# Kernel optimization log

Hardware: AMD Instinct MI355X
Metric: run time of the kernel (lower is better)

Reference implementation:

```python
import jax, jax.numpy as jnp
import numpy as np

LN_EPS = 1e-5  # torch LayerNorm default


def layer_norm(x, g, b):
    mu = jnp.mean(x, axis=-1, keepdims=True)
    var = jnp.mean((x - mu) ** 2, axis=-1, keepdims=True)
    return (x - mu) / jnp.sqrt(var + LN_EPS) * g + b


def setup_inputs() -> dict:
    key = jax.random.key(0)
    k0, k1 = jax.random.split(key, 2)
    B, C, N, T, D = 64, 2, 1024, 13, 256  # batch, in_dim, nodes, time_step+1, dim
    x = jax.random.normal(k0, (B, C, N, T), dtype=jnp.float32)
    conv_w = jax.random.normal(k1, (D, C, T), dtype=jnp.float32) * 0.05  # Conv2d kernel (1,T) squeezed
    conv_b = jnp.zeros((D,), dtype=jnp.float32)
    time_g = jnp.ones((D,), dtype=jnp.float32)
    time_b = jnp.zeros((D,), dtype=jnp.float32)
    static_g = jnp.ones((N,), dtype=jnp.float32)
    static_b = jnp.zeros((N,), dtype=jnp.float32)
    return {"x": x, "conv_w": conv_w, "conv_b": conv_b,
            "time_g": time_g, "time_b": time_b,
            "static_g": static_g, "static_b": static_b}


def reference(x, conv_w, conv_b, time_g, time_b, static_g, static_b):
    # Conv2d(in_dim, dim, kernel=(1, T)) on [B,C,N,T] -> [B,dim,N,1]; squeeze+transpose -> [B,N,dim]
    emb = jnp.einsum('bcnt,dct->bnd', x, conv_w) + conv_b
    emb = layer_norm(emb, time_g, time_b)  # [B, N, D]
    # Spearman rank correlation, batched (replaces Python loop over B)
    ranks = jnp.argsort(jnp.argsort(emb, axis=-1), axis=-1).astype(emb.dtype)  # [B,N,D]
    c = ranks - jnp.mean(ranks, axis=-1, keepdims=True)
    norm = jnp.sqrt(jnp.sum(c * c, axis=-1, keepdims=True))  # [B,N,1]
    corr = jnp.einsum('bnd,bmd->bnm', c, c)  # [B,N,N]
    adj = jnp.abs(corr / (norm * jnp.swapaxes(norm, -1, -2) + 1e-8))
    # LayerNorm over last (nodes) axis then ReLU
    return jax.nn.relu(layer_norm(adj, static_g, static_b))
```

## Files before the change

### kernel.cpp

```cpp
#include <hip/hip_runtime.h>


typedef __attribute__((ext_vector_type(4))) int i32x4;

__device__ __forceinline__ void load_lds16(const void* g, void* l) {
  __builtin_amdgcn_global_load_lds(
      (const __attribute__((address_space(1))) void*)g,
      (__attribute__((address_space(3))) void*)l, 16, 0, 0);
}

__global__ __launch_bounds__(256) void conv_rank_kernel(
    const float* __restrict__ x, const float* __restrict__ w,
    const float* __restrict__ cb, const float* __restrict__ tg,
    const float* __restrict__ tb, signed char* __restrict__ ranks)
{
  int grp = blockIdx.x;
  int b = grp >> 8;
  int n0 = (grp & 255) << 2;
  int tid = threadIdx.x;
  int wave = tid >> 6, lane = tid & 63;
  int row = b * 1024 + n0 + wave;

  __shared__ float xs[4][26];
  __shared__ unsigned int ws[4][256];

  if (tid < 104) {
    int c = tid / 52, rem = tid - c * 52;
    int r = rem / 13, t = rem - r * 13;
    xs[r][c * 13 + t] = x[((size_t)(b * 2 + c) * 1024 + n0 + r) * 13 + t];
  }
  __syncthreads();

  float accv[4];
  #pragma unroll
  for (int i = 0; i < 4; ++i) {
    int d = i * 64 + lane;
    const float2* wp = (const float2*)(w + d * 26);
    float a = cb[d];
    #pragma unroll
    for (int u = 0; u < 13; ++u) {
      float2 w2 = wp[u];
      a += w2.x * xs[wave][2 * u] + w2.y * xs[wave][2 * u + 1];
    }
    accv[i] = a;
  }

  float s1 = accv[0] + accv[1] + accv[2] + accv[3];
  float s2 = accv[0] * accv[0] + accv[1] * accv[1] +
             accv[2] * accv[2] + accv[3] * accv[3];
  #pragma unroll
  for (int o = 1; o < 64; o <<= 1) {
    s1 += __shfl_xor(s1, o);
    s2 += __shfl_xor(s2, o);
  }
  float mu = s1 * (1.0f / 256.0f);
  float var = s2 * (1.0f / 256.0f) - mu * mu;
  float rs = rsqrtf(var + 1e-5f);

  unsigned int key[4], okey[4];
  #pragma unroll
  for (int i = 0; i < 4; ++i) {
    int d = i * 64 + lane;
    float val = (accv[i] - mu) * rs * tg[d] + tb[d];
    unsigned int u = __float_as_uint(val);
    key[i] = (u & 0x80000000u) ? ~u : (u | 0x80000000u);
    okey[i] = key[i];
  }

  #pragma unroll
  for (int k = 2; k <= 256; k <<= 1) {
    #pragma unroll
    for (int j = k >> 1; j > 0; j >>= 1) {
      if (j < 64) {
        #pragma unroll
        for (int i = 0; i < 4; ++i) {
          unsigned int pk = __shfl_xor(key[i], j);
          int e = i * 64 + lane;
          bool km = ((e & j) == 0) == ((e & k) == 0);
          unsigned int mn = key[i] < pk ? key[i] : pk;
          unsigned int mx = key[i] < pk ? pk : key[i];
          key[i] = km ? mn : mx;
        }
      } else {
        int di = j >> 6;
        #pragma unroll
        for (int i = 0; i < 4; ++i) {
          if ((i & di) == 0) {
            int ip = i + di;
            int e = i * 64 + lane;
            bool up = ((e & k) == 0);
            unsigned int a = key[i], bb = key[ip];
            unsigned int mn = a < bb ? a : bb;
            unsigned int mx = a < bb ? bb : a;
            key[i]  = up ? mn : mx;
            key[ip] = up ? mx : mn;
          }
        }
      }
    }
  }

  #pragma unroll
  for (int i = 0; i < 4; ++i) ws[wave][i * 64 + lane] = key[i];
  __syncthreads();
  int pos[4] = {0, 0, 0, 0};
  #pragma unroll
  for (int s = 128; s > 0; s >>= 1) {
    #pragma unroll
    for (int i = 0; i < 4; ++i)
      pos[i] += (ws[wave][pos[i] + s - 1] < okey[i]) ? s : 0;
  }
  #pragma unroll
  for (int i = 0; i < 4; ++i)
    ranks[(size_t)row * 256 + i * 64 + lane] = (signed char)(pos[i] - 128);
}

__global__ __launch_bounds__(512, 4) void corr_ln_kernel(
    const signed char* __restrict__ ranks, const float* __restrict__ sg,
    const float* __restrict__ sb, float* __restrict__ out)
{
  int bid = blockIdx.x;
  int blk = (bid & 7) * 256 + (bid >> 3);
  int b  = blk >> 5;
  int n0 = (blk & 31) << 5;
  const signed char* R = ranks + (size_t)b * 1024 * 256;
  float* O = out + ((size_t)b * 1024 + n0) * 1024;

  __shared__ __align__(16) signed char As[8192];
  __shared__ __align__(16) signed char Bs[65536];
  __shared__ float red[8][64];
  __shared__ float stats[2][32];

  int tid = threadIdx.x;
  int wave = tid >> 6, lane = tid & 63;
  int fr = lane & 15, quad = lane >> 4;
  int cw = wave << 7;

  {
    int o = tid * 16;
    int kt_a = o >> 11, kq = (o >> 9) & 3, r32 = (o >> 4) & 31;
    load_lds16(R + (size_t)(n0 + r32) * 256 + kt_a * 64 + kq * 16, As + o);
  }

  i32x4 acc[2][8] = {};

  for (int kt = 0; kt < 4; ++kt) {
    #pragma unroll
    for (int i = 0; i < 8; ++i) {
      int o = i * 8192 + tid * 16;
      int kq = o >> 14, row = (o & 16383) >> 4;
      load_lds16(R + (size_t)row * 256 + kt * 64 + kq * 16, Bs + o);
    }
    __syncthreads();

    i32x4 af0 = *(const i32x4*)(As + kt * 2048 + quad * 512 + fr * 16);
    i32x4 af1 = *(const i32x4*)(As + kt * 2048 + quad * 512 + (16 + fr) * 16);
    #pragma unroll
    for (int ni = 0; ni < 8; ++ni) {
      i32x4 bf = *(const i32x4*)(Bs + quad * 16384 + (cw + ni * 16 + fr) * 16);
      acc[0][ni] = __builtin_amdgcn_mfma_i32_16x16x64_i8(af0, bf, acc[0][ni], 0, 0, 0);
      acc[1][ni] = __builtin_amdgcn_mfma_i32_16x16x64_i8(af1, bf, acc[1][ni], 0, 0, 0);
    }
    __syncthreads();
  }

  float nrm = sqrtf(1398080.0f);
  float inv_den = 1.0f / (nrm * nrm + 1e-8f);

  float s[2][4], q[2][4];
  #pragma unroll
  for (int mi = 0; mi < 2; ++mi) {
    #pragma unroll
    for (int v = 0; v < 4; ++v) {
      float ss = 0.0f, qq = 0.0f;
      #pragma unroll
      for (int ni = 0; ni < 8; ++ni) {
        float a = fabsf((float)(acc[mi][ni][v] - 64)) * inv_den;
        ss += a; qq += a * a;
      }
      #pragma unroll
      for (int o = 8; o > 0; o >>= 1) {
        ss += __shfl_xor(ss, o);
        qq += __shfl_xor(qq, o);
      }
      s[mi][v] = ss; q[mi][v] = qq;
    }
  }
  if (fr == 0) {
    #pragma unroll
    for (int mi = 0; mi < 2; ++mi)
      #pragma unroll
      for (int v = 0; v < 4; ++v) {
        int r = mi * 16 + quad * 4 + v;
        red[wave][r] = s[mi][v];
        red[wave][32 + r] = q[mi][v];
      }
  }
  __syncthreads();

  if (tid < 32) {
    float su = 0.0f, sq = 0.0f;
    #pragma unroll
    for (int ww = 0; ww < 8; ++ww) { su += red[ww][tid]; sq += red[ww][32 + tid]; }
    float mu = su * (1.0f / 1024.0f);
    float var = sq * (1.0f / 1024.0f) - mu * mu;
    stats[0][tid] = mu;
    stats[1][tid] = rsqrtf(var + 1e-5f);
  }
  __syncthreads();

  float gv[8], bv[8];
  #pragma unroll
  for (int ni = 0; ni < 8; ++ni) {
    int col = cw + ni * 16 + fr;
    gv[ni] = sg[col];
    bv[ni] = sb[col];
  }
  #pragma unroll
  for (int mi = 0; mi < 2; ++mi) {
    #pragma unroll
    for (int v = 0; v < 4; ++v) {
      int r = mi * 16 + quad * 4 + v;
      float mu = stats[0][r], rs = stats[1][r];
      float* orow = O + (size_t)r * 1024;
      #pragma unroll
      for (int ni = 0; ni < 8; ++ni) {
        float a = fabsf((float)(acc[mi][ni][v] - 64)) * inv_den;
        orow[cw + ni * 16 + fr] = fmaxf(0.0f, (a - mu) * rs * gv[ni] + bv[ni]);
      }
    }
  }
}

extern "C" void kernel_launch(void* const* d_in, const int* in_sizes, int n_in,
                              void* d_out, int out_size, void* d_ws, size_t ws_size,
                              hipStream_t stream) {
  const float* x  = (const float*)d_in[0];
  const float* w  = (const float*)d_in[1];
  const float* cb = (const float*)d_in[2];
  const float* tg = (const float*)d_in[3];
  const float* tb = (const float*)d_in[4];
  const float* sg = (const float*)d_in[5];
  const float* sb = (const float*)d_in[6];
  float* out = (float*)d_out;
  signed char* ranks = (signed char*)d_ws;

  conv_rank_kernel<<<16384, 256, 0, stream>>>(x, w, cb, tg, tb, ranks);
  corr_ln_kernel<<<2048, 512, 0, stream>>>(ranks, sg, sb, out);
}
```

Measured before the change: 529.9 us.

## Sort key-index pairs to scatter ranks directly and swizzle LDS tile layouts

The rank kernel now packs each key with its original index into a 64-bit value and bitonic-sorts the pairs. After sorting, each thread writes the rank straight to the original position, which removes the LDS staging, the barrier and the binary-search pass. The cost is 64-bit shuffles and compares throughout the sort, and scattered byte stores. The correlation kernel changes the As/Bs shared-memory tiles to a row-major layout with an XOR swizzle, so global loads are more contiguous per row and LDS reads hit fewer bank conflicts.

New measurement: 501.7 us. 1.06x faster.

```diff
diff --git a/kernel.cpp b/kernel.cpp
--- a/kernel.cpp
+++ b/kernel.cpp
@@ -22,7 +22,6 @@
   int row = b * 1024 + n0 + wave;
 
   __shared__ float xs[4][26];
-  __shared__ unsigned int ws[4][256];
 
   if (tid < 104) {
     int c = tid / 52, rem = tid - c * 52;
@@ -57,14 +56,14 @@
   float var = s2 * (1.0f / 256.0f) - mu * mu;
   float rs = rsqrtf(var + 1e-5f);
 
-  unsigned int key[4], okey[4];
+  unsigned long long kv[4];
   #pragma unroll
   for (int i = 0; i < 4; ++i) {
     int d = i * 64 + lane;
     float val = (accv[i] - mu) * rs * tg[d] + tb[d];
     unsigned int u = __float_as_uint(val);
-    key[i] = (u & 0x80000000u) ? ~u : (u | 0x80000000u);
-    okey[i] = key[i];
+    unsigned int key = (u & 0x80000000u) ? ~u : (u | 0x80000000u);
+    kv[i] = ((unsigned long long)key << 32) | (unsigned int)d;
   }
 
   #pragma unroll
@@ -74,12 +73,12 @@
       if (j < 64) {
         #pragma unroll
         for (int i = 0; i < 4; ++i) {
-          unsigned int pk = __shfl_xor(key[i], j);
+          unsigned long long p = __shfl_xor(kv[i], j);
           int e = i * 64 + lane;
           bool km = ((e & j) == 0) == ((e & k) == 0);
-          unsigned int mn = key[i] < pk ? key[i] : pk;
-          unsigned int mx = key[i] < pk ? pk : key[i];
-          key[i] = km ? mn : mx;
+          unsigned long long mn = kv[i] < p ? kv[i] : p;
+          unsigned long long mx = kv[i] < p ? p : kv[i];
+          kv[i] = km ? mn : mx;
         }
       } else {
         int di = j >> 6;
@@ -89,30 +88,23 @@
             int ip = i + di;
             int e = i * 64 + lane;
             bool up = ((e & k) == 0);
-            unsigned int a = key[i], bb = key[ip];
-            unsigned int mn = a < bb ? a : bb;
-            unsigned int mx = a < bb ? bb : a;
-            key[i]  = up ? mn : mx;
-            key[ip] = up ? mx : mn;
+            unsigned long long a = kv[i], bb = kv[ip];
+            unsigned long long mn = a < bb ? a : bb;
+            unsigned long long mx = a < bb ? bb : a;
+            kv[i]  = up ? mn : mx;
+            kv[ip] = up ? mx : mn;
           }
         }
       }
     }
   }
 
-  #pragma unroll
-  for (int i = 0; i < 4; ++i) ws[wave][i * 64 + lane] = key[i];
-  __syncthreads();
-  int pos[4] = {0, 0, 0, 0};
-  #pragma unroll
-  for (int s = 128; s > 0; s >>= 1) {
-    #pragma unroll
-    for (int i = 0; i < 4; ++i)
-      pos[i] += (ws[wave][pos[i] + s - 1] < okey[i]) ? s : 0;
-  }
-  #pragma unroll
-  for (int i = 0; i < 4; ++i)
-    ranks[(size_t)row * 256 + i * 64 + lane] = (signed char)(pos[i] - 128);
+  signed char* rr = ranks + (size_t)row * 256;
+  #pragma unroll
+  for (int i = 0; i < 4; ++i) {
+    int e = i * 64 + lane;
+    rr[kv[i] & 255] = (signed char)(e - 128);
+  }
 }
 
 __global__ __launch_bounds__(512, 4) void corr_ln_kernel(
@@ -126,8 +118,8 @@
   const signed char* R = ranks + (size_t)b * 1024 * 256;
   float* O = out + ((size_t)b * 1024 + n0) * 1024;
 
-  __shared__ __align__(16) signed char As[8192];
-  __shared__ __align__(16) signed char Bs[65536];
+  __shared__ __align__(16) signed char As[32 * 256];
+  __shared__ __align__(16) signed char Bs[1024 * 64];
   __shared__ float red[8][64];
   __shared__ float stats[2][32];
 
@@ -137,9 +129,9 @@
   int cw = wave << 7;
 
   {
-    int o = tid * 16;
-    int kt_a = o >> 11, kq = (o >> 9) & 3, r32 = (o >> 4) & 31;
-    load_lds16(R + (size_t)(n0 + r32) * 256 + kt_a * 64 + kq * 16, As + o);
+    int r = tid >> 4, cp = tid & 15;
+    int c = cp ^ (r & 7);
+    load_lds16(R + (size_t)(n0 + r) * 256 + c * 16, As + tid * 16);
   }
 
   i32x4 acc[2][8] = {};
@@ -147,17 +139,20 @@
   for (int kt = 0; kt < 4; ++kt) {
     #pragma unroll
     for (int i = 0; i < 8; ++i) {
-      int o = i * 8192 + tid * 16;
-      int kq = o >> 14, row = (o & 16383) >> 4;
-      load_lds16(R + (size_t)row * 256 + kt * 64 + kq * 16, Bs + o);
+      int r = i * 128 + (tid >> 2);
+      int q = (tid & 3) ^ (r & 3);
+      load_lds16(R + (size_t)r * 256 + kt * 64 + q * 16,
+                 Bs + i * 8192 + tid * 16);
     }
     __syncthreads();
 
-    i32x4 af0 = *(const i32x4*)(As + kt * 2048 + quad * 512 + fr * 16);
-    i32x4 af1 = *(const i32x4*)(As + kt * 2048 + quad * 512 + (16 + fr) * 16);
+    int csw = ((kt * 4 + quad) ^ (fr & 7)) << 4;
+    i32x4 af0 = *(const i32x4*)(As + fr * 256 + csw);
+    i32x4 af1 = *(const i32x4*)(As + (16 + fr) * 256 + csw);
     #pragma unroll
     for (int ni = 0; ni < 8; ++ni) {
-      i32x4 bf = *(const i32x4*)(Bs + quad * 16384 + (cw + ni * 16 + fr) * 16);
+      int rowb = cw + ni * 16 + fr;
+      i32x4 bf = *(const i32x4*)(Bs + rowb * 64 + ((quad ^ (rowb & 3)) << 4));
       acc[0][ni] = __builtin_amdgcn_mfma_i32_16x16x64_i8(af0, bf, acc[0][ni], 0, 0, 0);
       acc[1][ni] = __builtin_amdgcn_mfma_i32_16x16x64_i8(af1, bf, acc[1][ni], 0, 0, 0);
     }
```

## Double-buffer per-wave B tiles with swizzled LDS layout in corr kernel

Applied to the files above, without the earlier changes.

The correlation kernel now gives each wave its own double-buffered B tile in LDS and prefetches the next k-slice while computing the current one. It waits on vmcnt instead of block-wide barriers inside the k loop. A and B tiles use XOR-swizzled LDS layouts to avoid bank conflicts. Launch bounds drop to 2 blocks per CU to fit the larger shared footprint (~136KB), which may reduce occupancy.

Result: faster. 470.5 us (-11.2%).

```diff
diff --git a/kernel.cpp b/kernel.cpp
--- a/kernel.cpp
+++ b/kernel.cpp
@@ -115,7 +115,7 @@
     ranks[(size_t)row * 256 + i * 64 + lane] = (signed char)(pos[i] - 128);
 }
 
-__global__ __launch_bounds__(512, 4) void corr_ln_kernel(
+__global__ __launch_bounds__(512, 2) void corr_ln_kernel(
     const signed char* __restrict__ ranks, const float* __restrict__ sg,
     const float* __restrict__ sb, float* __restrict__ out)
 {
@@ -126,8 +126,8 @@
   const signed char* R = ranks + (size_t)b * 1024 * 256;
   float* O = out + ((size_t)b * 1024 + n0) * 1024;
 
-  __shared__ __align__(16) signed char As[8192];
-  __shared__ __align__(16) signed char Bs[65536];
+  __shared__ __align__(16) signed char As[32 * 256];
+  __shared__ __align__(16) signed char Bs[8][2][8192];
   __shared__ float red[8][64];
   __shared__ float stats[2][32];
 
@@ -137,32 +137,51 @@
   int cw = wave << 7;
 
   {
-    int o = tid * 16;
-    int kt_a = o >> 11, kq = (o >> 9) & 3, r32 = (o >> 4) & 31;
-    load_lds16(R + (size_t)(n0 + r32) * 256 + kt_a * 64 + kq * 16, As + o);
-  }
+    int r = tid >> 4, cp = tid & 15;
+    int c = cp ^ (r & 7);
+    load_lds16(R + (size_t)(n0 + r) * 256 + c * 16, As + tid * 16);
+  }
+
+  signed char* myB = &Bs[wave][0][0];
+  #define STAGE_B(kt, p)                                                      \
+    {                                                                         \
+      _Pragma("unroll")                                                       \
+      for (int i = 0; i < 8; ++i) {                                           \
+        int r = cw + i * 16 + (lane >> 2);                                    \
+        int q = (lane & 3) ^ (r & 3);                                         \
+        load_lds16(R + (size_t)r * 256 + (kt) * 64 + q * 16,                  \
+                   myB + (p) * 8192 + i * 1024 + lane * 16);                  \
+      }                                                                       \
+    }
+
+  STAGE_B(0, 0);
+  __syncthreads();
 
   i32x4 acc[2][8] = {};
 
+  #pragma unroll
   for (int kt = 0; kt < 4; ++kt) {
-    #pragma unroll
-    for (int i = 0; i < 8; ++i) {
-      int o = i * 8192 + tid * 16;
-      int kq = o >> 14, row = (o & 16383) >> 4;
-      load_lds16(R + (size_t)row * 256 + kt * 64 + kq * 16, Bs + o);
-    }
-    __syncthreads();
-
-    i32x4 af0 = *(const i32x4*)(As + kt * 2048 + quad * 512 + fr * 16);
-    i32x4 af1 = *(const i32x4*)(As + kt * 2048 + quad * 512 + (16 + fr) * 16);
+    if (kt < 3) {
+      STAGE_B(kt + 1, (kt + 1) & 1);
+      asm volatile("s_waitcnt vmcnt(8)" ::: "memory");
+    } else {
+      asm volatile("s_waitcnt vmcnt(0)" ::: "memory");
+    }
+    __builtin_amdgcn_sched_barrier(0);
+
+    const signed char* buf = myB + (kt & 1) * 8192;
+    int csw = ((kt * 4 + quad) ^ (fr & 7)) << 4;
+    i32x4 af0 = *(const i32x4*)(As + fr * 256 + csw);
+    i32x4 af1 = *(const i32x4*)(As + (16 + fr) * 256 + csw);
+    int bsw = (quad ^ (fr & 3)) << 4;
     #pragma unroll
     for (int ni = 0; ni < 8; ++ni) {
-      i32x4 bf = *(const i32x4*)(Bs + quad * 16384 + (cw + ni * 16 + fr) * 16);
+      i32x4 bf = *(const i32x4*)(buf + (ni * 16 + fr) * 64 + bsw);
       acc[0][ni] = __builtin_amdgcn_mfma_i32_16x16x64_i8(af0, bf, acc[0][ni], 0, 0, 0);
       acc[1][ni] = __builtin_amdgcn_mfma_i32_16x16x64_i8(af1, bf, acc[1][ni], 0, 0, 0);
     }
-    __syncthreads();
-  }
+  }
+  #undef STAGE_B
 
   float nrm = sqrtf(1398080.0f);
   float inv_den = 1.0f / (nrm * nrm + 1e-8f);
```
